# Kernel tuning notes

Measured on AMD Instinct MI355X. Metric: run time of the kernel, lower is better.

## Reference

```python
import jax, jax.numpy as jnp
import numpy as np

T, B, N, E, NF, L = 4, 8, 5000, 80000, 16, 3


def setup_inputs() -> dict:
    key = jax.random.key(0)
    ks = jax.random.split(key, 12)
    xs = jax.random.normal(ks[0], (T, B, N, 3), jnp.float32)
    vs = jax.random.normal(ks[1], (T, B, N, 3), jnp.float32)
    charges = jax.random.uniform(ks[2], (B * N, 1), jnp.float32)
    edge_src = jax.random.randint(ks[3], (E,), 0, N)
    edge_dst = jax.random.randint(ks[4], (E,), 0, N)
    theta = jax.random.uniform(ks[5], (1, T), jnp.float32, -1.0, 1.0)  # uniform_(-1,1)
    W_embed = jax.random.normal(ks[6], (1, NF), jnp.float32) * 0.5
    W1 = jax.random.normal(ks[7], (L, 2 * NF + 1, NF), jnp.float32) / jnp.sqrt(2.0 * NF + 1)
    b1 = jnp.zeros((L, NF), jnp.float32)
    W2 = jax.random.normal(ks[8], (L, NF, NF), jnp.float32) / jnp.sqrt(float(NF))
    b2 = jnp.zeros((L, NF), jnp.float32)
    Wv = jax.random.normal(ks[9], (L, NF, 1), jnp.float32) * 0.1
    return dict(xs=xs, vs=vs, charges=charges, edge_src=edge_src, edge_dst=edge_dst,
                theta=theta, W_embed=W_embed, W1=W1, b1=b1, W2=W2, b2=b2, Wv=Wv)


def reference(xs, vs, charges, edge_src, edge_dst, theta, W_embed, W1, b1, W2, b2, Wv):
    T_, B_, N_, _ = xs.shape
    # node scalar features ('f' / type-0) initialized from charges
    h0 = jax.nn.relu(charges.reshape(B_, N_, 1) @ W_embed)  # [B, N, NF]

    def graph_step(x, v, h):
        # x, v: [N,3]; h: [N,NF]. Equivariant message passing with edge rel-pos gather.
        d = x[edge_dst] - x[edge_src]                      # [E,3]  (edata['d'])
        d2 = jnp.sum(d * d, axis=-1, keepdims=True)        # [E,1]  invariant edge feature
        vec = v                                            # type-1 ('vel') channel
        for l in range(L):
            feat = jnp.concatenate([h[edge_src], h[edge_dst], d2], axis=-1)  # [E,2NF+1]
            m = jax.nn.relu(feat @ W1[l] + b1[l])                            # [E,NF]
            agg = jax.ops.segment_sum(m, edge_dst, num_segments=N_)          # [N,NF]
            h = h + jax.nn.relu(agg @ W2[l] + b2[l])
            # equivariant vector update: scatter d-weighted messages
            vec = vec + jax.ops.segment_sum(d * (m @ Wv[l]), edge_dst, num_segments=N_)
        return vec + x  # module returns out + xs

    step_b = jax.vmap(graph_step)                                  # over batch
    out = jax.vmap(lambda x, v: step_b(x, v, h0))(xs, vs)          # [T,B,N,3]
    x = out.reshape(T_, B_ * N_, 3)                                # step's view(-1, 3)
    x_hat = jnp.einsum('ij,jkt->ikt', jax.nn.softmax(theta, axis=1), x)
    return x_hat.squeeze(0)  # [B*N, 3] since num_future == 1
```

## Files before the change

kernel.cpp:

```cpp
#include <hip/hip_runtime.h>
#include <hip/hip_bf16.h>

constexpr int T_ = 4;
constexpr int B_ = 8;
constexpr int N_ = 5000;
constexpr int E_ = 80000;
constexpr int TBN = T_ * B_ * N_;
constexpr int NXCD = 8;

constexpr int NPB = 64;
constexpr int CH  = (N_ + NPB - 1) / NPB;
constexpr int GRP = T_ * B_ / NXCD;
constexpr int LB  = NXCD * CH * GRP;
constexpr int EB  = (E_ + 255) / 256;
constexpr int IB  = TBN / 256;


__device__ __forceinline__ unsigned bf16pack2(float lo, float hi) {
    unsigned ul = (__float_as_uint(lo) + 0x8000u) >> 16;
    unsigned uh = (__float_as_uint(hi) + 0x8000u) & 0xffff0000u;
    return uh | ul;
}
__device__ __forceinline__ void bf16unpack2(unsigned u, float& lo, float& hi) {
    lo = __uint_as_float(u << 16);
    hi = __uint_as_float(u & 0xffff0000u);
}

__global__ __launch_bounds__(1024) void k_build1(
        const int* __restrict__ edge_dst, int* __restrict__ row_start,
        int* __restrict__ cursor) {
    __shared__ int sdeg[5120];
    __shared__ int ssum[1024];
    const int tid = threadIdx.x;
    for (int i = tid; i < 5120; i += 1024) sdeg[i] = 0;
    __syncthreads();
    for (int e = tid; e < E_; e += 1024) atomicAdd(&sdeg[edge_dst[e]], 1);
    __syncthreads();
    const int base = tid * 5;
    int loc = 0;
#pragma unroll
    for (int i = 0; i < 5; ++i) { int ix = base + i; if (ix < N_) loc += sdeg[ix]; }
    ssum[tid] = loc;
    __syncthreads();
    for (int off = 1; off < 1024; off <<= 1) {
        int v = 0;
        if (tid >= off) v = ssum[tid - off];
        __syncthreads();
        if (tid >= off) ssum[tid] += v;
        __syncthreads();
    }
    int run = ssum[tid] - loc;
#pragma unroll
    for (int i = 0; i < 5; ++i) {
        int ix = base + i;
        if (ix < N_) { row_start[ix] = run; run += sdeg[ix]; }
    }
    if (tid == 1023) row_start[N_] = ssum[1023];
    for (int i = tid; i < N_; i += 1024) cursor[i] = 0;
}

__global__ void k_build2(const int* __restrict__ src, const int* __restrict__ dst,
                         const int* __restrict__ row_start, int* __restrict__ cursor,
                         int* __restrict__ csr_src,
                         const float* __restrict__ xs, const float* __restrict__ vs,
                         const float* __restrict__ charges,
                         float4* __restrict__ rec0, float4* __restrict__ rec1,
                         float* __restrict__ vec) {
    const int bid = blockIdx.x;
    const int tid = threadIdx.x;
    if (bid < EB) {
        int e = bid * 256 + tid;
        if (e < E_) {
            int d = dst[e];
            int pos = atomicAdd(&cursor[d], 1);
            csr_src[row_start[d] + pos] = src[e];
        }
    } else {
        int g = (bid - EB) * 256 + tid;
        int tb = g / N_;
        int n  = g - tb * N_;
        int b  = tb % B_;
        float c = charges[b * N_ + n];
        float4 xc = make_float4(xs[3*(size_t)g], xs[3*(size_t)g+1], xs[3*(size_t)g+2], c);
        rec0[(size_t)g * 3 + 2] = xc;
        rec1[(size_t)g * 3 + 2] = xc;
        vec[3*(size_t)g+0] = vs[3*(size_t)g+0];
        vec[3*(size_t)g+1] = vs[3*(size_t)g+1];
        vec[3*(size_t)g+2] = vs[3*(size_t)g+2];
    }
}

template <int LYR, bool HAS_NEXT>
__global__ __launch_bounds__(256, 4) void k_layer(
        const float4* __restrict__ rec_in, float4* __restrict__ rec_out,
        const float* __restrict__ W_embed,
        const float* __restrict__ W1, const float* __restrict__ b1,
        const float* __restrict__ W2, const float* __restrict__ b2,
        const float* __restrict__ Wv,
        const int* __restrict__ row_start, const int* __restrict__ csr_src,
        float* __restrict__ h, unsigned* __restrict__ gd,
        float* __restrict__ vec) {
    __shared__ float s_w1e[16], s_wv[16], s_b2[16], s_b1[16], s_b1n[16];
    __shared__ float s_W2[256];
    __shared__ float s_W1sn[256];
    __shared__ float s_W1dn[256];
    __shared__ float s_P[16], s_Q[16], s_rwe[16];
    const int tid = threadIdx.x;
    if (tid < 16) {
        s_w1e[tid] = W1[LYR * 528 + 512 + tid];
        s_wv[tid]  = Wv[LYR * 16 + tid];
        s_b2[tid]  = b2[LYR * 16 + tid];
        s_b1[tid]  = b1[LYR * 16 + tid];
        if (HAS_NEXT) s_b1n[tid] = b1[(LYR + 1) * 16 + tid];
    }
    s_W2[tid] = W2[LYR * 256 + tid];
    if (HAS_NEXT) {
        s_W1sn[tid] = W1[(LYR + 1) * 528 + tid];
        s_W1dn[tid] = W1[(LYR + 1) * 528 + 256 + tid];
    }
    if (LYR == 0 && tid < 16) {
        float accP = 0.0f, accQ = 0.0f;
        for (int j = 0; j < 16; ++j) {
            float r = fmaxf(W_embed[j], 0.0f);
            accP += r * W1[j * 16 + tid];
            accQ += r * W1[256 + j * 16 + tid];
        }
        s_P[tid] = accP; s_Q[tid] = accQ;
        s_rwe[tid] = fmaxf(W_embed[tid], 0.0f);
    }
    __syncthreads();

    const int bid   = blockIdx.x;
    const int xcd   = bid & 7;
    const int j     = bid >> 3;
    const int tb    = xcd + NXCD * (j / CH);
    const int chunk = j % CH;
    const int node  = chunk * NPB + (tid >> 2);
    const int q     = tid & 3;
    if (node >= N_) return;

    const int g = tb * N_ + node;
    const size_t nb = (size_t)tb * N_;
    const uint4* r4 = (const uint4*)rec_in;

    const float4 xn = rec_in[(size_t)g * 3 + 2];
    const float c0 = xn.w;

    float gdn[16];
    if (LYR == 0) {
#pragma unroll
        for (int f = 0; f < 16; ++f) gdn[f] = c0 * s_Q[f] + s_b1[f];
    } else {
        const uint4* gdp = (const uint4*)gd + (size_t)g * 2;
        uint4 da = gdp[0], db = gdp[1];
        bf16unpack2(da.x, gdn[0], gdn[1]);  bf16unpack2(da.y, gdn[2], gdn[3]);
        bf16unpack2(da.z, gdn[4], gdn[5]);  bf16unpack2(da.w, gdn[6], gdn[7]);
        bf16unpack2(db.x, gdn[8], gdn[9]);  bf16unpack2(db.y, gdn[10], gdn[11]);
        bf16unpack2(db.z, gdn[12], gdn[13]); bf16unpack2(db.w, gdn[14], gdn[15]);
    }

    float agg[16];
#pragma unroll
    for (int f = 0; f < 16; ++f) agg[f] = 0.0f;
    float av0 = 0.0f, av1 = 0.0f, av2 = 0.0f;

    const int rs = row_start[node];
    const int re = row_start[node + 1];

    int e = rs + q;
    bool have = e < re;
    int s = have ? csr_src[e] : 0;
    size_t si = nb + (size_t)s;
    float4 xc = rec_in[si * 3 + 2];
    uint4  ga, gb;
    if (LYR != 0) { ga = r4[si * 3]; gb = r4[si * 3 + 1]; }

    while (have) {
        int e2 = e + 4;
        bool have2 = e2 < re;
        int s2 = have2 ? csr_src[e2] : 0;
        size_t si2 = nb + (size_t)s2;
        float4 xc2 = rec_in[si2 * 3 + 2];
        uint4  ga2, gb2;
        if (LYR != 0) { ga2 = r4[si2 * 3]; gb2 = r4[si2 * 3 + 1]; }

        float d0 = xn.x - xc.x;
        float d1 = xn.y - xc.y;
        float d2v = xn.z - xc.z;
        float dd = d0*d0 + d1*d1 + d2v*d2v;

        float gsf[16];
        if (LYR == 0) {
            float cs = xc.w;
#pragma unroll
            for (int f = 0; f < 16; ++f) gsf[f] = cs * s_P[f];
        } else {
            bf16unpack2(ga.x, gsf[0], gsf[1]);  bf16unpack2(ga.y, gsf[2], gsf[3]);
            bf16unpack2(ga.z, gsf[4], gsf[5]);  bf16unpack2(ga.w, gsf[6], gsf[7]);
            bf16unpack2(gb.x, gsf[8], gsf[9]);  bf16unpack2(gb.y, gsf[10], gsf[11]);
            bf16unpack2(gb.z, gsf[12], gsf[13]); bf16unpack2(gb.w, gsf[14], gsf[15]);
        }

        float sval = 0.0f;
#pragma unroll
        for (int f = 0; f < 16; ++f) {
            float mv = fmaxf(__builtin_fmaf(dd, s_w1e[f], gdn[f]) + gsf[f], 0.0f);
            if (HAS_NEXT) agg[f] += mv;
            sval = __builtin_fmaf(mv, s_wv[f], sval);
        }
        av0 = __builtin_fmaf(d0, sval, av0);
        av1 = __builtin_fmaf(d1, sval, av1);
        av2 = __builtin_fmaf(d2v, sval, av2);

        e = e2; have = have2; xc = xc2; ga = ga2; gb = gb2;
    }

    av0 += __shfl_xor(av0, 1); av0 += __shfl_xor(av0, 2);
    av1 += __shfl_xor(av1, 1); av1 += __shfl_xor(av1, 2);
    av2 += __shfl_xor(av2, 1); av2 += __shfl_xor(av2, 2);

    if (q < 3) {
        float myav = (q == 0) ? av0 : ((q == 1) ? av1 : av2);
        vec[(size_t)g * 3 + q] += myav;
    }

    if (HAS_NEXT) {
#pragma unroll
        for (int f = 0; f < 16; ++f) {
            agg[f] += __shfl_xor(agg[f], 1);
            agg[f] += __shfl_xor(agg[f], 2);
        }

        float hq[4];
        if (LYR == 0) {
#pragma unroll
            for (int k = 0; k < 4; ++k) hq[k] = c0 * s_rwe[q * 4 + k];
        } else {
            float4 hv = ((const float4*)h)[(size_t)g * 4 + q];
            hq[0] = hv.x; hq[1] = hv.y; hq[2] = hv.z; hq[3] = hv.w;
        }

        float acc[4];
#pragma unroll
        for (int k = 0; k < 4; ++k) acc[k] = s_b2[q * 4 + k];
#pragma unroll
        for (int jj = 0; jj < 16; ++jj) {
            float aj = agg[jj];
#pragma unroll
            for (int k = 0; k < 4; ++k)
                acc[k] = __builtin_fmaf(aj, s_W2[jj * 16 + q * 4 + k], acc[k]);
        }
#pragma unroll
        for (int k = 0; k < 4; ++k) hq[k] += fmaxf(acc[k], 0.0f);

        const int lane = tid & 63;
        const int lbase = lane & ~3;
        float hfull[16];
#pragma unroll
        for (int sq = 0; sq < 4; ++sq) {
#pragma unroll
            for (int k = 0; k < 4; ++k)
                hfull[sq * 4 + k] = __shfl(hq[k], lbase + sq, 64);
        }

        float gso[4], gdo[4];
#pragma unroll
        for (int k = 0; k < 4; ++k) { gso[k] = 0.0f; gdo[k] = s_b1n[q * 4 + k]; }
#pragma unroll
        for (int jj = 0; jj < 16; ++jj) {
            float hj = hfull[jj];
#pragma unroll
            for (int k = 0; k < 4; ++k) {
                gso[k] = __builtin_fmaf(hj, s_W1sn[jj * 16 + q * 4 + k], gso[k]);
                gdo[k] = __builtin_fmaf(hj, s_W1dn[jj * 16 + q * 4 + k], gdo[k]);
            }
        }

        ((float4*)h)[(size_t)g * 4 + q] = make_float4(hq[0], hq[1], hq[2], hq[3]);
        ((uint2*)rec_out)[(size_t)g * 6 + q] =
            make_uint2(bf16pack2(gso[0], gso[1]), bf16pack2(gso[2], gso[3]));
        ((uint2*)gd)[(size_t)g * 4 + q] =
            make_uint2(bf16pack2(gdo[0], gdo[1]), bf16pack2(gdo[2], gdo[3]));
    }
}

__global__ void k_final(const float* __restrict__ xs, const float* __restrict__ vec,
                        const float* __restrict__ theta, float* __restrict__ out) {
    int g = blockIdx.x * 256 + threadIdx.x;
    if (g >= B_ * N_) return;
    float t0 = theta[0], t1 = theta[1], t2 = theta[2], t3 = theta[3];
    float mx = fmaxf(fmaxf(t0, t1), fmaxf(t2, t3));
    float e0 = expf(t0 - mx), e1 = expf(t1 - mx), e2 = expf(t2 - mx), e3 = expf(t3 - mx);
    float is = 1.0f / (e0 + e1 + e2 + e3);
    float w[4] = {e0 * is, e1 * is, e2 * is, e3 * is};

    int b = g / N_;
    int n = g - b * N_;
    float o0 = 0.0f, o1 = 0.0f, o2 = 0.0f;
#pragma unroll
    for (int t = 0; t < 4; ++t) {
        size_t idx = ((size_t)(t * B_ + b) * N_ + n) * 3;
        o0 += w[t] * (vec[idx+0] + xs[idx+0]);
        o1 += w[t] * (vec[idx+1] + xs[idx+1]);
        o2 += w[t] * (vec[idx+2] + xs[idx+2]);
    }
    out[(size_t)g*3+0] = o0;
    out[(size_t)g*3+1] = o1;
    out[(size_t)g*3+2] = o2;
}

extern "C" void kernel_launch(void* const* d_in, const int* in_sizes, int n_in,
                              void* d_out, int out_size, void* d_ws, size_t ws_size,
                              hipStream_t stream) {
    const float* xs       = (const float*)d_in[0];
    const float* vs       = (const float*)d_in[1];
    const float* charges  = (const float*)d_in[2];
    const int*   edge_src = (const int*)d_in[3];
    const int*   edge_dst = (const int*)d_in[4];
    const float* theta    = (const float*)d_in[5];
    const float* W_embed  = (const float*)d_in[6];
    const float* W1       = (const float*)d_in[7];
    const float* b1       = (const float*)d_in[8];
    const float* W2       = (const float*)d_in[9];
    const float* b2       = (const float*)d_in[10];
    const float* Wv       = (const float*)d_in[11];
    float* out = (float*)d_out;

    char* w = (char*)d_ws;
    size_t off = 0;
    auto take = [&](size_t bytes) {
        size_t o = off;
        off = (off + bytes + 255) & ~(size_t)255;
        return o;
    };
    int*      cursor    = (int*)(w + take((size_t)N_ * 4));
    int*      row_start = (int*)(w + take((size_t)(N_ + 1) * 4));
    int*      csr_src   = (int*)(w + take((size_t)E_ * 4));
    float4*   rec0      = (float4*)(w + take((size_t)TBN * 48));
    float4*   rec1      = (float4*)(w + take((size_t)TBN * 48));
    float*    h         = (float*)(w + take((size_t)TBN * 16 * 4));
    unsigned* gd        = (unsigned*)(w + take((size_t)TBN * 32));
    float*    vec       = (float*)(w + take((size_t)TBN * 3 * 4));
    (void)ws_size;

    k_build1<<<1, 1024, 0, stream>>>(edge_dst, row_start, cursor);
    k_build2<<<EB + IB, 256, 0, stream>>>(edge_src, edge_dst, row_start, cursor, csr_src,
                                          xs, vs, charges, rec0, rec1, vec);

    k_layer<0, true ><<<LB, 256, 0, stream>>>(rec0, rec1, W_embed, W1, b1, W2, b2, Wv,
                                              row_start, csr_src, h, gd, vec);
    k_layer<1, true ><<<LB, 256, 0, stream>>>(rec1, rec0, W_embed, W1, b1, W2, b2, Wv,
                                              row_start, csr_src, h, gd, vec);
    k_layer<2, false><<<LB, 256, 0, stream>>>(rec0, nullptr, W_embed, W1, b1, W2, b2, Wv,
                                              row_start, csr_src, h, gd, vec);

    const int fb = (B_ * N_ + 255) / 256;
    k_final<<<fb, 256, 0, stream>>>(xs, vec, theta, out);
}
```

Before: 121.7 us.

## Split each edge's 16 features across two lanes, using 8 threads per node

Each node is now handled by 8 threads instead of 4. The threads form 4 edge-parallel pairs, and each pair splits the 16 message features into two halves of 8. This halves the per-thread register arrays and the gathered bytes per lane, so occupancy and latency hiding should improve. The cost is an extra cross-lane shuffle per edge to combine the partial scalar, more shuffles when reducing agg, and half as many nodes per block.

```diff
diff --git a/kernel.cpp b/kernel.cpp
--- a/kernel.cpp
+++ b/kernel.cpp
@@ -8,7 +8,7 @@
 constexpr int TBN = T_ * B_ * N_;
 constexpr int NXCD = 8;
 
-constexpr int NPB = 64;
+constexpr int NPB = 32;
 constexpr int CH  = (N_ + NPB - 1) / NPB;
 constexpr int GRP = T_ * B_ / NXCD;
 constexpr int LB  = NXCD * CH * GRP;
@@ -135,8 +135,11 @@
     const int j     = bid >> 3;
     const int tb    = xcd + NXCD * (j / CH);
     const int chunk = j % CH;
-    const int node  = chunk * NPB + (tid >> 2);
-    const int q     = tid & 3;
+    const int o     = tid & 7;
+    const int node  = chunk * NPB + (tid >> 3);
+    const int half  = o & 1;
+    const int pr    = o >> 1;
+    const int hb    = half * 8;
     if (node >= N_) return;
 
     const int g = tb * N_ + node;
@@ -146,34 +149,31 @@
     const float4 xn = rec_in[(size_t)g * 3 + 2];
     const float c0 = xn.w;
 
-    float gdn[16];
+    float gdn[8];
     if (LYR == 0) {
 #pragma unroll
-        for (int f = 0; f < 16; ++f) gdn[f] = c0 * s_Q[f] + s_b1[f];
+        for (int k = 0; k < 8; ++k) gdn[k] = c0 * s_Q[hb + k] + s_b1[hb + k];
     } else {
-        const uint4* gdp = (const uint4*)gd + (size_t)g * 2;
-        uint4 da = gdp[0], db = gdp[1];
+        uint4 da = ((const uint4*)gd)[(size_t)g * 2 + half];
         bf16unpack2(da.x, gdn[0], gdn[1]);  bf16unpack2(da.y, gdn[2], gdn[3]);
         bf16unpack2(da.z, gdn[4], gdn[5]);  bf16unpack2(da.w, gdn[6], gdn[7]);
-        bf16unpack2(db.x, gdn[8], gdn[9]);  bf16unpack2(db.y, gdn[10], gdn[11]);
-        bf16unpack2(db.z, gdn[12], gdn[13]); bf16unpack2(db.w, gdn[14], gdn[15]);
-    }
-
-    float agg[16];
-#pragma unroll
-    for (int f = 0; f < 16; ++f) agg[f] = 0.0f;
+    }
+
+    float agg[8];
+#pragma unroll
+    for (int k = 0; k < 8; ++k) agg[k] = 0.0f;
     float av0 = 0.0f, av1 = 0.0f, av2 = 0.0f;
 
     const int rs = row_start[node];
     const int re = row_start[node + 1];
 
-    int e = rs + q;
+    int e = rs + pr;
     bool have = e < re;
     int s = have ? csr_src[e] : 0;
     size_t si = nb + (size_t)s;
     float4 xc = rec_in[si * 3 + 2];
-    uint4  ga, gb;
-    if (LYR != 0) { ga = r4[si * 3]; gb = r4[si * 3 + 1]; }
+    uint4  ga;
+    if (LYR != 0) ga = r4[si * 3 + half];
 
     while (have) {
         int e2 = e + 4;
@@ -181,106 +181,103 @@
         int s2 = have2 ? csr_src[e2] : 0;
         size_t si2 = nb + (size_t)s2;
         float4 xc2 = rec_in[si2 * 3 + 2];
-        uint4  ga2, gb2;
-        if (LYR != 0) { ga2 = r4[si2 * 3]; gb2 = r4[si2 * 3 + 1]; }
+        uint4  ga2;
+        if (LYR != 0) ga2 = r4[si2 * 3 + half];
 
         float d0 = xn.x - xc.x;
         float d1 = xn.y - xc.y;
         float d2v = xn.z - xc.z;
         float dd = d0*d0 + d1*d1 + d2v*d2v;
 
-        float gsf[16];
+        float gsf[8];
         if (LYR == 0) {
             float cs = xc.w;
 #pragma unroll
-            for (int f = 0; f < 16; ++f) gsf[f] = cs * s_P[f];
+            for (int k = 0; k < 8; ++k) gsf[k] = cs * s_P[hb + k];
         } else {
             bf16unpack2(ga.x, gsf[0], gsf[1]);  bf16unpack2(ga.y, gsf[2], gsf[3]);
             bf16unpack2(ga.z, gsf[4], gsf[5]);  bf16unpack2(ga.w, gsf[6], gsf[7]);
-            bf16unpack2(gb.x, gsf[8], gsf[9]);  bf16unpack2(gb.y, gsf[10], gsf[11]);
-            bf16unpack2(gb.z, gsf[12], gsf[13]); bf16unpack2(gb.w, gsf[14], gsf[15]);
         }
 
         float sval = 0.0f;
 #pragma unroll
-        for (int f = 0; f < 16; ++f) {
-            float mv = fmaxf(__builtin_fmaf(dd, s_w1e[f], gdn[f]) + gsf[f], 0.0f);
-            if (HAS_NEXT) agg[f] += mv;
-            sval = __builtin_fmaf(mv, s_wv[f], sval);
-        }
+        for (int k = 0; k < 8; ++k) {
+            float mv = fmaxf(__builtin_fmaf(dd, s_w1e[hb + k], gdn[k]) + gsf[k], 0.0f);
+            if (HAS_NEXT) agg[k] += mv;
+            sval = __builtin_fmaf(mv, s_wv[hb + k], sval);
+        }
+        sval += __shfl_xor(sval, 1);
         av0 = __builtin_fmaf(d0, sval, av0);
         av1 = __builtin_fmaf(d1, sval, av1);
         av2 = __builtin_fmaf(d2v, sval, av2);
 
-        e = e2; have = have2; xc = xc2; ga = ga2; gb = gb2;
-    }
-
-    av0 += __shfl_xor(av0, 1); av0 += __shfl_xor(av0, 2);
-    av1 += __shfl_xor(av1, 1); av1 += __shfl_xor(av1, 2);
-    av2 += __shfl_xor(av2, 1); av2 += __shfl_xor(av2, 2);
-
-    if (q < 3) {
-        float myav = (q == 0) ? av0 : ((q == 1) ? av1 : av2);
-        vec[(size_t)g * 3 + q] += myav;
+        e = e2; have = have2; xc = xc2; ga = ga2;
+    }
+
+    av0 += __shfl_xor(av0, 2); av0 += __shfl_xor(av0, 4);
+    av1 += __shfl_xor(av1, 2); av1 += __shfl_xor(av1, 4);
+    av2 += __shfl_xor(av2, 2); av2 += __shfl_xor(av2, 4);
+
+    if (o < 3) {
+        float myav = (o == 0) ? av0 : ((o == 1) ? av1 : av2);
+        vec[(size_t)g * 3 + o] += myav;
     }
 
     if (HAS_NEXT) {
 #pragma unroll
-        for (int f = 0; f < 16; ++f) {
-            agg[f] += __shfl_xor(agg[f], 1);
-            agg[f] += __shfl_xor(agg[f], 2);
-        }
-
-        float hq[4];
+        for (int k = 0; k < 8; ++k) {
+            agg[k] += __shfl_xor(agg[k], 2);
+            agg[k] += __shfl_xor(agg[k], 4);
+        }
+        float aggO[8];
+#pragma unroll
+        for (int k = 0; k < 8; ++k) aggO[k] = __shfl_xor(agg[k], 1);
+        const int j0 = hb;
+        const int j1 = 8 - hb;
+
+        float hq0, hq1;
         if (LYR == 0) {
-#pragma unroll
-            for (int k = 0; k < 4; ++k) hq[k] = c0 * s_rwe[q * 4 + k];
+            hq0 = c0 * s_rwe[o * 2];
+            hq1 = c0 * s_rwe[o * 2 + 1];
         } else {
-            float4 hv = ((const float4*)h)[(size_t)g * 4 + q];
-            hq[0] = hv.x; hq[1] = hv.y; hq[2] = hv.z; hq[3] = hv.w;
-        }
-
-        float acc[4];
-#pragma unroll
-        for (int k = 0; k < 4; ++k) acc[k] = s_b2[q * 4 + k];
-#pragma unroll
-        for (int jj = 0; jj < 16; ++jj) {
-            float aj = agg[jj];
-#pragma unroll
-            for (int k = 0; k < 4; ++k)
-                acc[k] = __builtin_fmaf(aj, s_W2[jj * 16 + q * 4 + k], acc[k]);
-        }
-#pragma unroll
-        for (int k = 0; k < 4; ++k) hq[k] += fmaxf(acc[k], 0.0f);
+            float2 hv = ((const float2*)h)[(size_t)g * 8 + o];
+            hq0 = hv.x; hq1 = hv.y;
+        }
+
+        float a0 = s_b2[o * 2], a1 = s_b2[o * 2 + 1];
+#pragma unroll
+        for (int k = 0; k < 8; ++k) {
+            a0 = __builtin_fmaf(agg[k],  s_W2[(j0 + k) * 16 + o * 2],     a0);
+            a1 = __builtin_fmaf(agg[k],  s_W2[(j0 + k) * 16 + o * 2 + 1], a1);
+            a0 = __builtin_fmaf(aggO[k], s_W2[(j1 + k) * 16 + o * 2],     a0);
+            a1 = __builtin_fmaf(aggO[k], s_W2[(j1 + k) * 16 + o * 2 + 1], a1);
+        }
+        hq0 += fmaxf(a0, 0.0f);
+        hq1 += fmaxf(a1, 0.0f);
 
         const int lane = tid & 63;
-        const int lbase = lane & ~3;
+        const int lbase = lane & ~7;
         float hfull[16];
 #pragma unroll
-        for (int sq = 0; sq < 4; ++sq) {
-#pragma unroll
-            for (int k = 0; k < 4; ++k)
-                hfull[sq * 4 + k] = __shfl(hq[k], lbase + sq, 64);
-        }
-
-        float gso[4], gdo[4];
-#pragma unroll
-        for (int k = 0; k < 4; ++k) { gso[k] = 0.0f; gdo[k] = s_b1n[q * 4 + k]; }
+        for (int sq = 0; sq < 8; ++sq) {
+            hfull[sq * 2]     = __shfl(hq0, lbase + sq, 64);
+            hfull[sq * 2 + 1] = __shfl(hq1, lbase + sq, 64);
+        }
+
+        float gs0 = 0.0f, gs1 = 0.0f;
+        float gd0 = s_b1n[o * 2], gd1 = s_b1n[o * 2 + 1];
 #pragma unroll
         for (int jj = 0; jj < 16; ++jj) {
             float hj = hfull[jj];
-#pragma unroll
-            for (int k = 0; k < 4; ++k) {
-                gso[k] = __builtin_fmaf(hj, s_W1sn[jj * 16 + q * 4 + k], gso[k]);
-                gdo[k] = __builtin_fmaf(hj, s_W1dn[jj * 16 + q * 4 + k], gdo[k]);
-            }
-        }
-
-        ((float4*)h)[(size_t)g * 4 + q] = make_float4(hq[0], hq[1], hq[2], hq[3]);
-        ((uint2*)rec_out)[(size_t)g * 6 + q] =
-            make_uint2(bf16pack2(gso[0], gso[1]), bf16pack2(gso[2], gso[3]));
-        ((uint2*)gd)[(size_t)g * 4 + q] =
-            make_uint2(bf16pack2(gdo[0], gdo[1]), bf16pack2(gdo[2], gdo[3]));
+            gs0 = __builtin_fmaf(hj, s_W1sn[jj * 16 + o * 2],     gs0);
+            gs1 = __builtin_fmaf(hj, s_W1sn[jj * 16 + o * 2 + 1], gs1);
+            gd0 = __builtin_fmaf(hj, s_W1dn[jj * 16 + o * 2],     gd0);
+            gd1 = __builtin_fmaf(hj, s_W1dn[jj * 16 + o * 2 + 1], gd1);
+        }
+
+        ((float2*)h)[(size_t)g * 8 + o] = make_float2(hq0, hq1);
+        ((unsigned*)rec_out)[(size_t)g * 12 + o] = bf16pack2(gs0, gs1);
+        ((unsigned*)gd)[(size_t)g * 8 + o]       = bf16pack2(gd0, gd1);
     }
 }
 
```

Measured after the change: 122.2 us. No clear change (+0.4%).
